# Kernel optimization log

Measured on AMD Instinct MI355X. Metric: run time of the kernel, lower is better.

Reference implementation:

```python
import jax, jax.numpy as jnp
import numpy as np

D_MODEL = 256
N_HEADS = 8
D_K = D_MODEL // N_HEADS
FFN_DIM = 1024
LN_EPS = 1e-5


def _layernorm(x, g, b):
    mu = jnp.mean(x, axis=-1, keepdims=True)
    var = jnp.var(x, axis=-1, keepdims=True)
    return (x - mu) * jax.lax.rsqrt(var + LN_EPS) * g + b


def setup_inputs() -> dict:
    key = jax.random.key(0)
    ks = jax.random.split(key, 16)
    B, Q, K = 2, 2048, 64
    s = 1.0 / np.sqrt(D_MODEL)
    inp = {
        "target_queries": jax.random.normal(ks[0], (B, Q, D_MODEL), jnp.float32),
        "sampled_features": jax.random.normal(ks[1], (B, Q, K, D_MODEL), jnp.float32),
        "Wq": jax.random.normal(ks[2], (D_MODEL, D_MODEL), jnp.float32) * s,
        "bq": jnp.zeros((D_MODEL,), jnp.float32),
        "Wk": jax.random.normal(ks[3], (D_MODEL, D_MODEL), jnp.float32) * s,
        "bk": jnp.zeros((D_MODEL,), jnp.float32),
        "Wv": jax.random.normal(ks[4], (D_MODEL, D_MODEL), jnp.float32) * s,
        "bv": jnp.zeros((D_MODEL,), jnp.float32),
        "Wo": jax.random.normal(ks[5], (D_MODEL, D_MODEL), jnp.float32) * s,
        "bo": jnp.zeros((D_MODEL,), jnp.float32),
        "g1": jnp.ones((D_MODEL,), jnp.float32),
        "beta1": jnp.zeros((D_MODEL,), jnp.float32),
        "g2": jnp.ones((D_MODEL,), jnp.float32),
        "beta2": jnp.zeros((D_MODEL,), jnp.float32),
        "W1": jax.random.normal(ks[6], (D_MODEL, FFN_DIM), jnp.float32) * s,
        "b1": jnp.zeros((FFN_DIM,), jnp.float32),
        "W2": jax.random.normal(ks[7], (FFN_DIM, D_MODEL), jnp.float32) * (1.0 / np.sqrt(FFN_DIM)),
        "b2": jnp.zeros((D_MODEL,), jnp.float32),
    }
    return inp


def reference(target_queries, sampled_features, Wq, bq, Wk, bk, Wv, bv, Wo, bo,
              g1, beta1, g2, beta2, W1, b1, W2, b2):
    B, Q, C = target_queries.shape
    K = sampled_features.shape[2]
    H, Dk = N_HEADS, D_K

    # pre-norm + projections (dropout is identity at eval)
    qn = _layernorm(target_queries, g1, beta1)
    q = (qn @ Wq + bq).reshape(B, Q, H, Dk).transpose(0, 2, 1, 3)            # bhqd
    k = (sampled_features @ Wk + bk).reshape(B, Q, K, H, Dk).transpose(0, 3, 1, 2, 4)  # bhqkd
    v = (sampled_features @ Wv + bv).reshape(B, Q, K, H, Dk).transpose(0, 3, 1, 2, 4)  # bhqkd

    # per-query gathered K/V attention
    scores = jnp.einsum('bhqd,bhqkd->bhqk', q, k) / np.sqrt(Dk).astype(np.float32)
    attn_weights = jax.nn.softmax(scores, axis=-1)                            # (B,H,Q,K)
    attn_out = jnp.einsum('bhqk,bhqkd->bhqd', attn_weights, v)
    attn_out = attn_out.transpose(0, 2, 1, 3).reshape(B, Q, C)
    attn_out = attn_out @ Wo + bo

    x = target_queries + attn_out

    # FFN with pre-norm residual (exact erf GELU, as torch default)
    h = _layernorm(x, g2, beta2)
    h = jax.nn.gelu(h @ W1 + b1, approximate=False) @ W2 + b2
    out = x + h
    return out, attn_weights
```

## Files before the change

### kernel.cpp

```cpp
#include <hip/hip_runtime.h>
#include <math.h>

#define QTOT 2048

using bf16x8 = __attribute__((ext_vector_type(8))) short;
using f32x4  = __attribute__((ext_vector_type(4))) float;

static __device__ __forceinline__ short f2bf(float f) {
    union { float f; unsigned u; } v; v.f = f;
    unsigned r = v.u + 0x7fffu + ((v.u >> 16) & 1u);
    return (short)(r >> 16);
}
static __device__ __forceinline__ unsigned cvt_pk(float a, float b) {
    unsigned r;
    asm("v_cvt_pk_bf16_f32 %0, %1, %2" : "=v"(r) : "v"(a), "v"(b));
    return r;
}
static __device__ __forceinline__ bf16x8 pack8(float a0, float a1, float a2, float a3,
                                               float a4, float a5, float a6, float a7) {
    union { unsigned u[4]; bf16x8 v; } z;
    z.u[0] = cvt_pk(a0, a1); z.u[1] = cvt_pk(a2, a3);
    z.u[2] = cvt_pk(a4, a5); z.u[3] = cvt_pk(a6, a7);
    return z.v;
}

__global__ void wconv(const float* __restrict__ Wq, const float* __restrict__ Wk,
                      const float* __restrict__ Wo, const float* __restrict__ Wv,
                      const float* __restrict__ W1, const float* __restrict__ W2,
                      short* __restrict__ WqP, short* __restrict__ WkP,
                      short* __restrict__ WoP, short* __restrict__ WvP,
                      short* __restrict__ W1P, short* __restrict__ W2P) {
    int b = blockIdx.x, t = threadIdx.x;
    const float* W; short* P; int N, KK, ci; bool tr = false;
    if (b < 32)       { W = Wq; P = WqP; N = 256;  KK = 8;  ci = b * 256 + t; }
    else if (b < 64)  { W = Wk; P = WkP; N = 256;  KK = 8;  ci = (b - 32) * 256 + t; tr = true; }
    else if (b < 96)  { W = Wo; P = WoP; N = 256;  KK = 8;  ci = (b - 64) * 256 + t; }
    else if (b < 128) { W = Wv; P = WvP; N = 256;  KK = 8;  ci = (b - 96) * 256 + t; }
    else if (b < 256) { W = W1; P = W1P; N = 1024; KK = 8;  ci = (b - 128) * 256 + t; }
    else              { W = W2; P = W2P; N = 256;  KK = 32; ci = (b - 256) * 256 + t; }
    int cb = ci / (KK * 64);
    int rem = ci - cb * (KK * 64);
    int kk = rem >> 6, l = rem & 63;
    int lr = l & 15, lg = l >> 4;
    int n = cb * 16 + lr, k0 = kk * 32 + lg * 8;
    short pk[8];
    if (!tr) {
#pragma unroll
        for (int e = 0; e < 8; ++e) pk[e] = f2bf(W[(size_t)(k0 + e) * N + n]);
    } else {
#pragma unroll
        for (int e = 0; e < 8; ++e) pk[e] = f2bf(W[(size_t)n * 256 + (k0 + e)]);
    }
    *reinterpret_cast<bf16x8*>(P + (size_t)ci * 8) = *reinterpret_cast<bf16x8*>(pk);
}

__global__ void ln1z(const float* __restrict__ tq, const short* __restrict__ WqP,
                     const float* __restrict__ bq, const float* __restrict__ g1,
                     const float* __restrict__ be1, const short* __restrict__ WkP,
                     const float* __restrict__ bk, short* __restrict__ zf,
                     float* __restrict__ sbg) {
    __shared__ float xs[8 * 260];
    __shared__ float qs[8 * 260];
    int r0 = blockIdx.x * 8, t = threadIdx.x;
    int w = t >> 6, l = t & 63, lr = l & 15, lg = l >> 4;
#pragma unroll
    for (int it = 0; it < 8; ++it) xs[it * 260 + t] = tq[(size_t)(r0 + it) * 256 + t];
    __syncthreads();
#pragma unroll
    for (int i = 0; i < 2; ++i) {
        int r = w * 2 + i;
        float s = 0.f, s2 = 0.f;
        for (int j = l; j < 256; j += 64) { float x = xs[r * 260 + j]; s += x; s2 += x * x; }
#pragma unroll
        for (int m = 1; m < 64; m <<= 1) { s += __shfl_xor(s, m); s2 += __shfl_xor(s2, m); }
        float mu = s * (1.f / 256.f);
        float var = s2 * (1.f / 256.f) - mu * mu;
        float rstd = rsqrtf(var + 1e-5f);
        for (int j = l; j < 256; j += 64)
            xs[r * 260 + j] = (xs[r * 260 + j] - mu) * rstd * g1[j] + be1[j];
    }
    __syncthreads();
    f32x4 cq[4];
#pragma unroll
    for (int ni = 0; ni < 4; ++ni) cq[ni] = (f32x4){0.f, 0.f, 0.f, 0.f};
#pragma unroll
    for (int kk = 0; kk < 8; ++kk) {
        bf16x8 af = {0, 0, 0, 0, 0, 0, 0, 0};
        if (lr < 8) {
            const float* xp = &xs[lr * 260 + kk * 32 + lg * 8];
            af = pack8(xp[0], xp[1], xp[2], xp[3], xp[4], xp[5], xp[6], xp[7]);
        }
#pragma unroll
        for (int ni = 0; ni < 4; ++ni) {
            bf16x8 bf = *reinterpret_cast<const bf16x8*>(WqP + ((size_t)((w * 4 + ni) * 8 + kk) * 64 + l) * 8);
            cq[ni] = __builtin_amdgcn_mfma_f32_16x16x32_bf16(af, bf, cq[ni], 0, 0, 0);
        }
    }
    if (lg < 2) {
#pragma unroll
        for (int ni = 0; ni < 4; ++ni)
#pragma unroll
            for (int r = 0; r < 4; ++r) {
                int row = lg * 4 + r, col = (w * 4 + ni) * 16 + lr;
                qs[row * 260 + col] = cq[ni][r] + bq[col];
            }
    }
    __syncthreads();
    if (t < 64) {
        int r = t >> 3, h = t & 7;
        float s = 0.f;
        for (int d = 0; d < 32; ++d) s += qs[r * 260 + h * 32 + d] * bk[h * 32 + d];
        sbg[(size_t)(r0 + r) * 8 + h] = s;
    }
    f32x4 cz[4][4];
#pragma unroll
    for (int mi = 0; mi < 4; ++mi)
#pragma unroll
        for (int ni = 0; ni < 4; ++ni) cz[mi][ni] = (f32x4){0.f, 0.f, 0.f, 0.f};
#pragma unroll
    for (int kk = 0; kk < 8; ++kk) {
        bf16x8 am[4];
#pragma unroll
        for (int mi = 0; mi < 4; ++mi) {
            bf16x8 z = {0, 0, 0, 0, 0, 0, 0, 0};
            if ((lr & 7) == kk) {
                int rr = mi * 2 + (lr >> 3);
                const float* qp = &qs[rr * 260 + kk * 32 + lg * 8];
                z = pack8(qp[0], qp[1], qp[2], qp[3], qp[4], qp[5], qp[6], qp[7]);
            }
            am[mi] = z;
        }
#pragma unroll
        for (int ni = 0; ni < 4; ++ni) {
            bf16x8 bf = *reinterpret_cast<const bf16x8*>(WkP + ((size_t)((w * 4 + ni) * 8 + kk) * 64 + l) * 8);
#pragma unroll
            for (int mi = 0; mi < 4; ++mi)
                cz[mi][ni] = __builtin_amdgcn_mfma_f32_16x16x32_bf16(am[mi], bf, cz[mi][ni], 0, 0, 0);
        }
    }
#pragma unroll
    for (int mi = 0; mi < 4; ++mi)
#pragma unroll
        for (int ni = 0; ni < 4; ++ni)
#pragma unroll
            for (int r = 0; r < 4; ++r) {
                int mrow = mi * 16 + lg * 4 + r;
                int rr = mrow >> 3, hh = mrow & 7;
                int i = (w * 4 + ni) * 16 + lr;
                zf[(size_t)(r0 + rr) * 2048 + (i >> 3) * 64 + hh * 8 + (i & 7)] = f2bf(cz[mi][ni][r]);
            }
}

__launch_bounds__(256, 4)
__global__ void attn(const float* __restrict__ sf, const short* __restrict__ zf,
                     const float* __restrict__ sbg, const short* __restrict__ WvP,
                     const float* __restrict__ bv, short* __restrict__ aob,
                     float* __restrict__ attn_w) {
    __shared__ __align__(16) char arena[39040];
    char* Xb = arena;
    float* sp = reinterpret_cast<float*>(arena + 32768);
    char* Ub = arena + 34944;

    int bq = blockIdx.x, t = threadIdx.x;
    int w = t >> 6, l = t & 63, lr = l & 15, lg = l >> 4;
    const float* Xg = sf + (size_t)bq * 16384;

    float4 fa[16];
#pragma unroll
    for (int q = 0; q < 8; ++q) {
        int c = q * 256 + t;
        fa[2 * q]     = *reinterpret_cast<const float4*>(Xg + c * 8);
        fa[2 * q + 1] = *reinterpret_cast<const float4*>(Xg + c * 8 + 4);
    }
    bf16x8 zfr[8];
#pragma unroll
    for (int kk = 0; kk < 8; ++kk) {
        bf16x8 z = {0, 0, 0, 0, 0, 0, 0, 0};
        if (lr < 8)
            z = *reinterpret_cast<const bf16x8*>(zf + (size_t)bq * 2048 + ((size_t)((kk * 4 + lg) * 8 + lr)) * 8);
        zfr[kk] = z;
    }
#pragma unroll
    for (int q = 0; q < 8; ++q) {
        int c = q * 256 + t;
        int key = c >> 5, ch = (c & 31) * 8;
        int base = (key * 512 + ch * 2) ^ ((key & 7) << 4);
        *reinterpret_cast<bf16x8*>(Xb + base) =
            pack8(fa[2 * q].x, fa[2 * q].y, fa[2 * q].z, fa[2 * q].w,
                  fa[2 * q + 1].x, fa[2 * q + 1].y, fa[2 * q + 1].z, fa[2 * q + 1].w);
    }
    __syncthreads();

    f32x4 cs = {0.f, 0.f, 0.f, 0.f};
    {
        int key = w * 16 + lr;
        int swz = (key & 7) << 4;
#pragma unroll
        for (int kk = 0; kk < 8; ++kk) {
            int addr = (key * 512 + kk * 64 + lg * 16) ^ swz;
            bf16x8 xb = *reinterpret_cast<const bf16x8*>(Xb + addr);
            cs = __builtin_amdgcn_mfma_f32_16x16x32_bf16(zfr[kk], xb, cs, 0, 0, 0);
        }
    }
    if (lg < 2) {
#pragma unroll
        for (int r = 0; r < 4; ++r)
            sp[(lg * 4 + r) * 68 + w * 16 + lr] = cs[r];
    }
    __syncthreads();

    const float scale = 0.17677669529663687f;
    int b = bq >> 11, qq = bq & 2047;
#pragma unroll
    for (int hi = 0; hi < 2; ++hi) {
        int h = w * 2 + hi;
        float sbh = sbg[(size_t)bq * 8 + h];
        float s = (sp[h * 68 + l] + sbh) * scale;
        float m = s;
#pragma unroll
        for (int off = 1; off < 64; off <<= 1) m = fmaxf(m, __shfl_xor(m, off));
        float p = __expf(s - m);
        float sm = p;
#pragma unroll
        for (int off = 1; off < 64; off <<= 1) sm += __shfl_xor(sm, off);
        float P = p / sm;
        sp[h * 68 + l] = P;
        attn_w[(((size_t)b * 8 + h) * QTOT + qq) * 64 + l] = P;
    }
    __syncthreads();

    {
        int h = t >> 5, cg = t & 31;
        float acc[8];
#pragma unroll
        for (int e = 0; e < 8; ++e) acc[e] = 0.f;
#pragma unroll
        for (int k4 = 0; k4 < 16; ++k4) {
            float4 pv = *reinterpret_cast<const float4*>(&sp[h * 68 + k4 * 4]);
#pragma unroll
            for (int e = 0; e < 4; ++e) {
                int key = k4 * 4 + e;
                float P = (e == 0) ? pv.x : (e == 1) ? pv.y : (e == 2) ? pv.z : pv.w;
                int addr = (key * 512 + cg * 16) ^ ((key & 7) << 4);
                union { bf16x8 v; unsigned u[4]; } xv;
                xv.v = *reinterpret_cast<const bf16x8*>(Xb + addr);
#pragma unroll
                for (int d = 0; d < 4; ++d) {
                    union { unsigned u; float f; } lo, hi;
                    lo.u = xv.u[d] << 16;
                    hi.u = xv.u[d] & 0xffff0000u;
                    acc[2 * d]     += P * lo.f;
                    acc[2 * d + 1] += P * hi.f;
                }
            }
        }
        int ub = (h * 512 + cg * 16) ^ ((h & 7) << 4);
        *reinterpret_cast<bf16x8*>(Ub + ub) =
            pack8(acc[0], acc[1], acc[2], acc[3], acc[4], acc[5], acc[6], acc[7]);
    }
    __syncthreads();

    f32x4 co[4];
#pragma unroll
    for (int ni = 0; ni < 4; ++ni) co[ni] = (f32x4){0.f, 0.f, 0.f, 0.f};
#pragma unroll
    for (int kk = 0; kk < 8; ++kk) {
        bf16x8 ua = {0, 0, 0, 0, 0, 0, 0, 0};
        if (lr < 8) {
            int addr = (lr * 512 + kk * 64 + lg * 16) ^ ((lr & 7) << 4);
            ua = *reinterpret_cast<const bf16x8*>(Ub + addr);
        }
#pragma unroll
        for (int ni = 0; ni < 4; ++ni) {
            bf16x8 bf = *reinterpret_cast<const bf16x8*>(WvP + ((size_t)((w * 4 + ni) * 8 + kk) * 64 + l) * 8);
            co[ni] = __builtin_amdgcn_mfma_f32_16x16x32_bf16(ua, bf, co[ni], 0, 0, 0);
        }
    }
    if (lg < 2) {
#pragma unroll
        for (int ni = 0; ni < 4; ++ni) {
            int j = (w * 4 + ni) * 16 + lr;
            int h = j >> 5;
            if ((h >> 2) == lg)
                aob[(size_t)bq * 256 + j] = f2bf(co[ni][h & 3] + bv[j]);
        }
    }
}

__launch_bounds__(512, 1)
__global__ void tail(const short* __restrict__ aob, const float* __restrict__ tq,
                     const short* __restrict__ WoP, const float* __restrict__ bo,
                     const float* __restrict__ g2, const float* __restrict__ be2,
                     const short* __restrict__ W1P, const float* __restrict__ b1,
                     const short* __restrict__ W2P, const float* __restrict__ b2,
                     float* __restrict__ out) {
    __shared__ float xrow[16][260];
    __shared__ short xn[16][264];
    __shared__ short hs[16][1048];
    int r0 = blockIdx.x * 16, t = threadIdx.x;
    int w = t >> 6, l = t & 63, lr = l & 15, lg = l >> 4;

    f32x4 c[2];
#pragma unroll
    for (int ni = 0; ni < 2; ++ni) c[ni] = (f32x4){0.f, 0.f, 0.f, 0.f};
#pragma unroll
    for (int kk = 0; kk < 8; ++kk) {
        bf16x8 af = *reinterpret_cast<const bf16x8*>(aob + (size_t)(r0 + lr) * 256 + kk * 32 + lg * 8);
#pragma unroll
        for (int ni = 0; ni < 2; ++ni) {
            bf16x8 bf = *reinterpret_cast<const bf16x8*>(WoP + ((size_t)((w * 2 + ni) * 8 + kk) * 64 + l) * 8);
            c[ni] = __builtin_amdgcn_mfma_f32_16x16x32_bf16(af, bf, c[ni], 0, 0, 0);
        }
    }
#pragma unroll
    for (int ni = 0; ni < 2; ++ni) {
        int col = (w * 2 + ni) * 16 + lr;
        float bb = bo[col];
#pragma unroll
        for (int r = 0; r < 4; ++r) {
            int row = lg * 4 + r;
            xrow[row][col] = tq[(size_t)(r0 + row) * 256 + col] + c[ni][r] + bb;
        }
    }
    __syncthreads();

#pragma unroll
    for (int i = 0; i < 2; ++i) {
        int r = w * 2 + i;
        float s = 0.f, s2 = 0.f;
        for (int j = l; j < 256; j += 64) { float x = xrow[r][j]; s += x; s2 += x * x; }
#pragma unroll
        for (int m = 1; m < 64; m <<= 1) { s += __shfl_xor(s, m); s2 += __shfl_xor(s2, m); }
        float mu = s * (1.f / 256.f);
        float var = s2 * (1.f / 256.f) - mu * mu;
        float rstd = rsqrtf(var + 1e-5f);
        for (int j = l; j < 256; j += 64)
            xn[r][j] = f2bf((xrow[r][j] - mu) * rstd * g2[j] + be2[j]);
    }
    __syncthreads();

    bf16x8 af1[8];
#pragma unroll
    for (int kk = 0; kk < 8; ++kk)
        af1[kk] = *reinterpret_cast<const bf16x8*>(&xn[lr][kk * 32 + lg * 8]);
#pragma unroll
    for (int nt = 0; nt < 8; ++nt) {
        int cb = w * 8 + nt;
        f32x4 cc = {0.f, 0.f, 0.f, 0.f};
#pragma unroll
        for (int kk = 0; kk < 8; ++kk) {
            bf16x8 bf = *reinterpret_cast<const bf16x8*>(W1P + ((size_t)(cb * 8 + kk) * 64 + l) * 8);
            cc = __builtin_amdgcn_mfma_f32_16x16x32_bf16(af1[kk], bf, cc, 0, 0, 0);
        }
        int col = cb * 16 + lr;
        float bb = b1[col];
#pragma unroll
        for (int r = 0; r < 4; ++r) {
            int row = lg * 4 + r;
            float v = cc[r] + bb;
            float g = 0.5f * v * (1.f + erff(v * 0.7071067811865475f));
            hs[row][col] = f2bf(g);
        }
    }
    __syncthreads();

    f32x4 c2[2];
#pragma unroll
    for (int ni = 0; ni < 2; ++ni) c2[ni] = (f32x4){0.f, 0.f, 0.f, 0.f};
#pragma unroll
    for (int kk = 0; kk < 32; ++kk) {
        bf16x8 af = *reinterpret_cast<const bf16x8*>(&hs[lr][kk * 32 + lg * 8]);
#pragma unroll
        for (int ni = 0; ni < 2; ++ni) {
            bf16x8 bf = *reinterpret_cast<const bf16x8*>(W2P + ((size_t)((w * 2 + ni) * 32 + kk) * 64 + l) * 8);
            c2[ni] = __builtin_amdgcn_mfma_f32_16x16x32_bf16(af, bf, c2[ni], 0, 0, 0);
        }
    }
#pragma unroll
    for (int ni = 0; ni < 2; ++ni) {
        int col = (w * 2 + ni) * 16 + lr;
        float bb = b2[col];
#pragma unroll
        for (int r = 0; r < 4; ++r) {
            int row = lg * 4 + r;
            out[(size_t)(r0 + row) * 256 + col] = xrow[row][col] + c2[ni][r] + bb;
        }
    }
}

extern "C" void kernel_launch(void* const* d_in, const int* in_sizes, int n_in,
                              void* d_out, int out_size, void* d_ws, size_t ws_size,
                              hipStream_t stream) {
    const float* tq  = (const float*)d_in[0];
    const float* sf  = (const float*)d_in[1];
    const float* Wq  = (const float*)d_in[2];
    const float* bq  = (const float*)d_in[3];
    const float* Wk  = (const float*)d_in[4];
    const float* bk  = (const float*)d_in[5];
    const float* Wv  = (const float*)d_in[6];
    const float* bv  = (const float*)d_in[7];
    const float* Wo  = (const float*)d_in[8];
    const float* bo  = (const float*)d_in[9];
    const float* g1  = (const float*)d_in[10];
    const float* be1 = (const float*)d_in[11];
    const float* g2  = (const float*)d_in[12];
    const float* be2 = (const float*)d_in[13];
    const float* W1  = (const float*)d_in[14];
    const float* b1  = (const float*)d_in[15];
    const float* W2  = (const float*)d_in[16];
    const float* b2  = (const float*)d_in[17];

    char* wsb = (char*)d_ws;
    short* WqP = (short*)(wsb + 0);
    short* WkP = (short*)(wsb + 131072);
    short* WoP = (short*)(wsb + 262144);
    short* WvP = (short*)(wsb + 393216);
    short* W1P = (short*)(wsb + 524288);
    short* W2P = (short*)(wsb + 1048576);
    float* sbw = (float*)(wsb + 1572864);
    short* zf  = (short*)(wsb + 1703936);
    short* aob = (short*)(wsb + 18481152);

    float* outp   = (float*)d_out;
    float* attnwp = (float*)d_out + 1048576;

    wconv<<<384, 256, 0, stream>>>(Wq, Wk, Wo, Wv, W1, W2, WqP, WkP, WoP, WvP, W1P, W2P);
    ln1z<<<512, 256, 0, stream>>>(tq, WqP, bq, g1, be1, WkP, bk, zf, sbw);
    attn<<<4096, 256, 0, stream>>>(sf, zf, sbw, WvP, bv, aob, attnwp);
    tail<<<256, 512, 0, stream>>>(aob, tq, WoP, bo, g2, be2, W1P, b1, W2P, b2, outp);
}
```

Before: 132.0 us.

## Process four queries per attn block with register prefetch of next features

Each attn block now loops over four consecutive queries instead of handling one. The global loads of the next query's sampled features and z vectors are issued into registers during the current query's softmax and PV phases. They are written to shared memory after the Wv MFMA, so load latency overlaps with compute. The grid shrinks to a quarter of its previous size and launch bounds drop to 2 waves per EU, which trades occupancy-based latency hiding for explicit software pipelining.

```diff
diff --git a/kernel.cpp b/kernel.cpp
--- a/kernel.cpp
+++ b/kernel.cpp
@@ -151,7 +151,8 @@
             }
 }
 
-__launch_bounds__(256, 4)
+#define NB 4
+__launch_bounds__(256, 2)
 __global__ void attn(const float* __restrict__ sf, const short* __restrict__ zf,
                      const float* __restrict__ sbg, const short* __restrict__ WvP,
                      const float* __restrict__ bv, short* __restrict__ aob,
@@ -161,23 +162,25 @@
     float* sp = reinterpret_cast<float*>(arena + 32768);
     char* Ub = arena + 34944;
 
-    int bq = blockIdx.x, t = threadIdx.x;
+    int bq0 = blockIdx.x * NB, t = threadIdx.x;
     int w = t >> 6, l = t & 63, lr = l & 15, lg = l >> 4;
-    const float* Xg = sf + (size_t)bq * 16384;
 
     float4 fa[16];
-#pragma unroll
-    for (int q = 0; q < 8; ++q) {
-        int c = q * 256 + t;
-        fa[2 * q]     = *reinterpret_cast<const float4*>(Xg + c * 8);
-        fa[2 * q + 1] = *reinterpret_cast<const float4*>(Xg + c * 8 + 4);
+    {
+        const float* Xg = sf + (size_t)bq0 * 16384;
+#pragma unroll
+        for (int q = 0; q < 8; ++q) {
+            int c = q * 256 + t;
+            fa[2 * q]     = *reinterpret_cast<const float4*>(Xg + c * 8);
+            fa[2 * q + 1] = *reinterpret_cast<const float4*>(Xg + c * 8 + 4);
+        }
     }
     bf16x8 zfr[8];
 #pragma unroll
     for (int kk = 0; kk < 8; ++kk) {
         bf16x8 z = {0, 0, 0, 0, 0, 0, 0, 0};
         if (lr < 8)
-            z = *reinterpret_cast<const bf16x8*>(zf + (size_t)bq * 2048 + ((size_t)((kk * 4 + lg) * 8 + lr)) * 8);
+            z = *reinterpret_cast<const bf16x8*>(zf + (size_t)bq0 * 2048 + ((size_t)((kk * 4 + lg) * 8 + lr)) * 8);
         zfr[kk] = z;
     }
 #pragma unroll
@@ -191,99 +194,130 @@
     }
     __syncthreads();
 
-    f32x4 cs = {0.f, 0.f, 0.f, 0.f};
-    {
-        int key = w * 16 + lr;
-        int swz = (key & 7) << 4;
+    const float scale = 0.17677669529663687f;
+
+    for (int i = 0; i < NB; ++i) {
+        int bq = bq0 + i;
+        f32x4 cs = {0.f, 0.f, 0.f, 0.f};
+        {
+            int key = w * 16 + lr;
+            int swz = (key & 7) << 4;
+#pragma unroll
+            for (int kk = 0; kk < 8; ++kk) {
+                int addr = (key * 512 + kk * 64 + lg * 16) ^ swz;
+                bf16x8 xb = *reinterpret_cast<const bf16x8*>(Xb + addr);
+                cs = __builtin_amdgcn_mfma_f32_16x16x32_bf16(zfr[kk], xb, cs, 0, 0, 0);
+            }
+        }
+        if (lg < 2) {
+#pragma unroll
+            for (int r = 0; r < 4; ++r)
+                sp[(lg * 4 + r) * 68 + w * 16 + lr] = cs[r];
+        }
+        __syncthreads();
+
+        int b = bq >> 11, qq = bq & 2047;
+#pragma unroll
+        for (int hi = 0; hi < 2; ++hi) {
+            int h = w * 2 + hi;
+            float sbh = sbg[(size_t)bq * 8 + h];
+            float s = (sp[h * 68 + l] + sbh) * scale;
+            float m = s;
+#pragma unroll
+            for (int off = 1; off < 64; off <<= 1) m = fmaxf(m, __shfl_xor(m, off));
+            float p = __expf(s - m);
+            float sm = p;
+#pragma unroll
+            for (int off = 1; off < 64; off <<= 1) sm += __shfl_xor(sm, off);
+            float P = p / sm;
+            sp[h * 68 + l] = P;
+            attn_w[(((size_t)b * 8 + h) * QTOT + qq) * 64 + l] = P;
+        }
+
+        if (i + 1 < NB) {
+            const float* Xg2 = sf + (size_t)(bq + 1) * 16384;
+#pragma unroll
+            for (int q = 0; q < 8; ++q) {
+                int c = q * 256 + t;
+                fa[2 * q]     = *reinterpret_cast<const float4*>(Xg2 + c * 8);
+                fa[2 * q + 1] = *reinterpret_cast<const float4*>(Xg2 + c * 8 + 4);
+            }
+#pragma unroll
+            for (int kk = 0; kk < 8; ++kk) {
+                if (lr < 8)
+                    zfr[kk] = *reinterpret_cast<const bf16x8*>(zf + (size_t)(bq + 1) * 2048 + ((size_t)((kk * 4 + lg) * 8 + lr)) * 8);
+            }
+        }
+        __syncthreads();
+
+        {
+            int h = t >> 5, cg = t & 31;
+            float acc[8];
+#pragma unroll
+            for (int e = 0; e < 8; ++e) acc[e] = 0.f;
+#pragma unroll
+            for (int k4 = 0; k4 < 16; ++k4) {
+                float4 pv = *reinterpret_cast<const float4*>(&sp[h * 68 + k4 * 4]);
+#pragma unroll
+                for (int e = 0; e < 4; ++e) {
+                    int key = k4 * 4 + e;
+                    float P = (e == 0) ? pv.x : (e == 1) ? pv.y : (e == 2) ? pv.z : pv.w;
+                    int addr = (key * 512 + cg * 16) ^ ((key & 7) << 4);
+                    union { bf16x8 v; unsigned u[4]; } xv;
+                    xv.v = *reinterpret_cast<const bf16x8*>(Xb + addr);
+#pragma unroll
+                    for (int d = 0; d < 4; ++d) {
+                        union { unsigned u; float f; } lo, hi;
+                        lo.u = xv.u[d] << 16;
+                        hi.u = xv.u[d] & 0xffff0000u;
+                        acc[2 * d]     += P * lo.f;
+                        acc[2 * d + 1] += P * hi.f;
+                    }
+                }
+            }
+            int ub = (h * 512 + cg * 16) ^ ((h & 7) << 4);
+            *reinterpret_cast<bf16x8*>(Ub + ub) =
+                pack8(acc[0], acc[1], acc[2], acc[3], acc[4], acc[5], acc[6], acc[7]);
+        }
+        __syncthreads();
+
+        f32x4 co[4];
+#pragma unroll
+        for (int ni = 0; ni < 4; ++ni) co[ni] = (f32x4){0.f, 0.f, 0.f, 0.f};
 #pragma unroll
         for (int kk = 0; kk < 8; ++kk) {
-            int addr = (key * 512 + kk * 64 + lg * 16) ^ swz;
-            bf16x8 xb = *reinterpret_cast<const bf16x8*>(Xb + addr);
-            cs = __builtin_amdgcn_mfma_f32_16x16x32_bf16(zfr[kk], xb, cs, 0, 0, 0);
-        }
-    }
-    if (lg < 2) {
-#pragma unroll
-        for (int r = 0; r < 4; ++r)
-            sp[(lg * 4 + r) * 68 + w * 16 + lr] = cs[r];
-    }
-    __syncthreads();
-
-    const float scale = 0.17677669529663687f;
-    int b = bq >> 11, qq = bq & 2047;
-#pragma unroll
-    for (int hi = 0; hi < 2; ++hi) {
-        int h = w * 2 + hi;
-        float sbh = sbg[(size_t)bq * 8 + h];
-        float s = (sp[h * 68 + l] + sbh) * scale;
-        float m = s;
-#pragma unroll
-        for (int off = 1; off < 64; off <<= 1) m = fmaxf(m, __shfl_xor(m, off));
-        float p = __expf(s - m);
-        float sm = p;
-#pragma unroll
-        for (int off = 1; off < 64; off <<= 1) sm += __shfl_xor(sm, off);
-        float P = p / sm;
-        sp[h * 68 + l] = P;
-        attn_w[(((size_t)b * 8 + h) * QTOT + qq) * 64 + l] = P;
-    }
-    __syncthreads();
-
-    {
-        int h = t >> 5, cg = t & 31;
-        float acc[8];
-#pragma unroll
-        for (int e = 0; e < 8; ++e) acc[e] = 0.f;
-#pragma unroll
-        for (int k4 = 0; k4 < 16; ++k4) {
-            float4 pv = *reinterpret_cast<const float4*>(&sp[h * 68 + k4 * 4]);
-#pragma unroll
-            for (int e = 0; e < 4; ++e) {
-                int key = k4 * 4 + e;
-                float P = (e == 0) ? pv.x : (e == 1) ? pv.y : (e == 2) ? pv.z : pv.w;
-                int addr = (key * 512 + cg * 16) ^ ((key & 7) << 4);
-                union { bf16x8 v; unsigned u[4]; } xv;
-                xv.v = *reinterpret_cast<const bf16x8*>(Xb + addr);
-#pragma unroll
-                for (int d = 0; d < 4; ++d) {
-                    union { unsigned u; float f; } lo, hi;
-                    lo.u = xv.u[d] << 16;
-                    hi.u = xv.u[d] & 0xffff0000u;
-                    acc[2 * d]     += P * lo.f;
-                    acc[2 * d + 1] += P * hi.f;
-                }
-            }
-        }
-        int ub = (h * 512 + cg * 16) ^ ((h & 7) << 4);
-        *reinterpret_cast<bf16x8*>(Ub + ub) =
-            pack8(acc[0], acc[1], acc[2], acc[3], acc[4], acc[5], acc[6], acc[7]);
-    }
-    __syncthreads();
-
-    f32x4 co[4];
-#pragma unroll
-    for (int ni = 0; ni < 4; ++ni) co[ni] = (f32x4){0.f, 0.f, 0.f, 0.f};
-#pragma unroll
-    for (int kk = 0; kk < 8; ++kk) {
-        bf16x8 ua = {0, 0, 0, 0, 0, 0, 0, 0};
-        if (lr < 8) {
-            int addr = (lr * 512 + kk * 64 + lg * 16) ^ ((lr & 7) << 4);
-            ua = *reinterpret_cast<const bf16x8*>(Ub + addr);
-        }
-#pragma unroll
-        for (int ni = 0; ni < 4; ++ni) {
-            bf16x8 bf = *reinterpret_cast<const bf16x8*>(WvP + ((size_t)((w * 4 + ni) * 8 + kk) * 64 + l) * 8);
-            co[ni] = __builtin_amdgcn_mfma_f32_16x16x32_bf16(ua, bf, co[ni], 0, 0, 0);
-        }
-    }
-    if (lg < 2) {
-#pragma unroll
-        for (int ni = 0; ni < 4; ++ni) {
-            int j = (w * 4 + ni) * 16 + lr;
-            int h = j >> 5;
-            if ((h >> 2) == lg)
-                aob[(size_t)bq * 256 + j] = f2bf(co[ni][h & 3] + bv[j]);
-        }
+            bf16x8 ua = {0, 0, 0, 0, 0, 0, 0, 0};
+            if (lr < 8) {
+                int addr = (lr * 512 + kk * 64 + lg * 16) ^ ((lr & 7) << 4);
+                ua = *reinterpret_cast<const bf16x8*>(Ub + addr);
+            }
+#pragma unroll
+            for (int ni = 0; ni < 4; ++ni) {
+                bf16x8 bf = *reinterpret_cast<const bf16x8*>(WvP + ((size_t)((w * 4 + ni) * 8 + kk) * 64 + l) * 8);
+                co[ni] = __builtin_amdgcn_mfma_f32_16x16x32_bf16(ua, bf, co[ni], 0, 0, 0);
+            }
+        }
+        if (i + 1 < NB) {
+#pragma unroll
+            for (int q = 0; q < 8; ++q) {
+                int c = q * 256 + t;
+                int key = c >> 5, ch = (c & 31) * 8;
+                int base = (key * 512 + ch * 2) ^ ((key & 7) << 4);
+                *reinterpret_cast<bf16x8*>(Xb + base) =
+                    pack8(fa[2 * q].x, fa[2 * q].y, fa[2 * q].z, fa[2 * q].w,
+                          fa[2 * q + 1].x, fa[2 * q + 1].y, fa[2 * q + 1].z, fa[2 * q + 1].w);
+            }
+        }
+        if (lg < 2) {
+#pragma unroll
+            for (int ni = 0; ni < 4; ++ni) {
+                int j = (w * 4 + ni) * 16 + lr;
+                int h = j >> 5;
+                if ((h >> 2) == lg)
+                    aob[(size_t)bq * 256 + j] = f2bf(co[ni][h & 3] + bv[j]);
+            }
+        }
+        __syncthreads();
     }
 }
 
@@ -426,6 +460,6 @@
 
     wconv<<<384, 256, 0, stream>>>(Wq, Wk, Wo, Wv, W1, W2, WqP, WkP, WoP, WvP, W1P, W2P);
     ln1z<<<512, 256, 0, stream>>>(tq, WqP, bq, g1, be1, WkP, bk, zf, sbw);
-    attn<<<4096, 256, 0, stream>>>(sf, zf, sbw, WvP, bv, aob, attnwp);
+    attn<<<1024, 256, 0, stream>>>(sf, zf, sbw, WvP, bv, aob, attnwp);
     tail<<<256, 512, 0, stream>>>(aob, tq, WoP, bo, g2, be2, W1P, b1, W2P, b2, outp);
 }
```

Measured after the change: 159.3 us. 20.7% more time.
